# Optimization experiments

Hardware: AMD Instinct MI355X
Metric: run time of the kernel (lower is better)

Reference implementation:

```python
import jax, jax.numpy as jnp
import numpy as np

N_NODES = 100000
N_EDGES = 1600000
D_IN = 64
D_OUT = 64
ROW_WINDOW = 16  # TCGNN row-window size (metadata only)


def setup_inputs() -> dict:
    key = jax.random.key(0)
    ks = jax.random.split(key, 7)
    X = jax.random.normal(ks[0], (N_NODES, D_IN), dtype=jnp.float32)
    weights = jax.random.normal(ks[1], (D_IN, D_OUT), dtype=jnp.float32)
    # CSR row pointers: sorted offsets into the edge list, endpoints pinned.
    rp = jnp.sort(jax.random.randint(ks[2], (N_NODES + 1,), 0, N_EDGES, dtype=jnp.int32))
    row_pointers = rp.at[0].set(0).at[-1].set(N_EDGES)
    column_index = jax.random.randint(ks[3], (N_EDGES,), 0, N_NODES, dtype=jnp.int32)
    # TCGNN tiling metadata (does not affect the math; kept for signature fidelity)
    blockPartition = jax.random.randint(ks[4], (N_NODES // ROW_WINDOW,), 0, 8, dtype=jnp.int32)
    edgeToColumn = jax.random.randint(ks[5], (N_EDGES,), 0, N_NODES, dtype=jnp.int32)
    edgeToRow = jax.random.randint(ks[6], (N_EDGES,), 0, N_NODES, dtype=jnp.int32)
    return {
        "X": X,
        "weights": weights,
        "row_pointers": row_pointers,
        "column_index": column_index,
        "blockPartition": blockPartition,
        "edgeToColumn": edgeToColumn,
        "edgeToRow": edgeToRow,
    }


def reference(X, weights, row_pointers, column_index, blockPartition, edgeToColumn, edgeToRow):
    # TCGNN.forward == unweighted CSR SpMM: X_prime[i] = sum_{j in N(i)} X[j]
    n_edges = column_index.shape[0]
    # Map each edge position to its CSR row id.
    row_ids = jnp.searchsorted(row_pointers, jnp.arange(n_edges, dtype=row_pointers.dtype), side="right") - 1
    gathered = X[column_index]  # [n_edges, d_in] irregular gather
    X_prime = jax.ops.segment_sum(gathered, row_ids, num_segments=X.shape[0])  # [n_nodes, d_in]
    return X_prime @ weights  # dense GEMM [n_nodes, d_out]
```

## Files before the change

### kernel.cpp

```cpp
#include <hip/hip_runtime.h>
#include <cstdint>
#include <cstddef>

#define D 64

typedef float    f32x4 __attribute__((ext_vector_type(4)));
typedef short    s16x8 __attribute__((ext_vector_type(8)));
typedef uint32_t u32x4 __attribute__((ext_vector_type(4)));

__device__ __forceinline__ uint32_t rne_bf16(float f) {
    uint32_t x = __float_as_uint(f);
    return (x + 0x7fffu + ((x >> 16) & 1u)) >> 16;
}
__device__ __forceinline__ float bf16lo(uint32_t u) { return __uint_as_float(u << 16); }
__device__ __forceinline__ float bf16hi(uint32_t u) { return __uint_as_float(u & 0xffff0000u); }

__global__ __launch_bounds__(256) void xw_gemm_kernel(
    const float* __restrict__ X, const float* __restrict__ W,
    uint32_t* __restrict__ XWh, int n_nodes)
{
    const int lane = threadIdx.x & 63;
    const int n = lane & 15;
    const int q = lane >> 4;

    s16x8 Af[4][2];
#pragma unroll
    for (int c = 0; c < 4; ++c)
#pragma unroll
        for (int kb = 0; kb < 2; ++kb) {
            s16x8 af;
#pragma unroll
            for (int j = 0; j < 8; ++j) {
                const int k = kb * 32 + q * 8 + j;
                af[j] = (short)rne_bf16(W[k * D + c * 16 + n]);
            }
            Af[c][kb] = af;
        }

    const int n_tiles = (n_nodes + 15) / 16;
    const int gwave = (int)((blockIdx.x * blockDim.x + threadIdx.x) >> 6);
    const int nwaves = (int)((gridDim.x * blockDim.x) >> 6);

    for (int t = gwave; t < n_tiles; t += nwaves) {
        const int m0 = t * 16;
        int arow = m0 + n;
        if (arow >= n_nodes) arow = n_nodes - 1;
        const float* xp = X + (size_t)arow * D;

        s16x8 Bf[2];
#pragma unroll
        for (int kb = 0; kb < 2; ++kb) {
            const f32x4 x0 = __builtin_nontemporal_load((const f32x4*)(xp + kb * 32 + q * 8));
            const f32x4 x1 = __builtin_nontemporal_load((const f32x4*)(xp + kb * 32 + q * 8 + 4));
            s16x8 b;
            b[0] = (short)rne_bf16(x0.x); b[1] = (short)rne_bf16(x0.y);
            b[2] = (short)rne_bf16(x0.z); b[3] = (short)rne_bf16(x0.w);
            b[4] = (short)rne_bf16(x1.x); b[5] = (short)rne_bf16(x1.y);
            b[6] = (short)rne_bf16(x1.z); b[7] = (short)rne_bf16(x1.w);
            Bf[kb] = b;
        }

        const bool live = (m0 + n) < n_nodes;
#pragma unroll
        for (int c = 0; c < 4; ++c) {
            f32x4 z = {0.f, 0.f, 0.f, 0.f};
            z = __builtin_amdgcn_mfma_f32_16x16x32_bf16(Af[c][0], Bf[0], z, 0, 0, 0);
            z = __builtin_amdgcn_mfma_f32_16x16x32_bf16(Af[c][1], Bf[1], z, 0, 0, 0);
            if (live) {
                uint2 o;
                o.x = rne_bf16(z[0]) | (rne_bf16(z[1]) << 16);
                o.y = rne_bf16(z[2]) | (rne_bf16(z[3]) << 16);
                *(uint2*)(XWh + (size_t)(m0 + n) * 32 + c * 8 + q * 2) = o;
            }
        }
    }
}

__global__ __launch_bounds__(256) void gather1shot_kernel(
    const uint32_t* __restrict__ XWh, const int* __restrict__ rp,
    const int* __restrict__ ci, float* __restrict__ out, int n_nodes)
{
    const int lane = threadIdx.x & 63;
    const int o = lane >> 3;
    const int p = lane & 7;
    const int gw = (int)((blockIdx.x * blockDim.x + threadIdx.x) >> 6);
    const int row = __builtin_amdgcn_readfirstlane(gw);
    if (row >= n_nodes) return;

    const int e0 = rp[row];
    const int e1 = rp[row + 1];

    float acc[8] = {0, 0, 0, 0, 0, 0, 0, 0};

    int e = e0;
    while (e < e1) {
        const int rem = e1 - e;

        int idx[8];
        bool v[8];
#pragma unroll
        for (int t = 0; t < 8; ++t) {
            v[t] = (t * 8 + o) < rem;
            if (v[t]) idx[t] = ci[e + t * 8 + o];
        }
        u32x4 u[8];
#pragma unroll
        for (int t = 0; t < 8; ++t)
            if (v[t]) u[t] = *(const u32x4*)(XWh + (size_t)idx[t] * 32 + p * 4);
#pragma unroll
        for (int t = 0; t < 8; ++t) {
            if (v[t]) {
#pragma unroll
                for (int k = 0; k < 4; ++k) {
                    acc[2 * k]     += bf16lo(u[t][k]);
                    acc[2 * k + 1] += bf16hi(u[t][k]);
                }
            }
        }
        e += 64;
    }

#pragma unroll
    for (int j = 0; j < 8; ++j) {
        float vv = acc[j];
        vv += __shfl_xor(vv, 8, 64);
        vv += __shfl_xor(vv, 16, 64);
        vv += __shfl_xor(vv, 32, 64);
        acc[j] = vv;
    }
    if (lane < 8) {
        f32x4 w0 = {acc[0], acc[1], acc[2], acc[3]};
        f32x4 w1 = {acc[4], acc[5], acc[6], acc[7]};
        *(f32x4*)(out + (size_t)row * D + p * 8)     = w0;
        *(f32x4*)(out + (size_t)row * D + p * 8 + 4) = w1;
    }
}

__global__ __launch_bounds__(256) void fused_kernel(
    const float* __restrict__ X, const float* __restrict__ W,
    const int* __restrict__ rp, const int* __restrict__ ci,
    float* __restrict__ out, int n_nodes)
{
    __shared__ float Wl[D * D];
    for (int i = threadIdx.x; i < D * D; i += 256) Wl[i] = W[i];
    __syncthreads();

    const int lane = threadIdx.x & 63;
    const int gwave = (int)((blockIdx.x * blockDim.x + threadIdx.x) >> 6);
    const int nwaves = (int)((gridDim.x * blockDim.x) >> 6);

    for (int row = gwave; row < n_nodes; row += nwaves) {
        int e0 = rp[row];
        int e1 = rp[row + 1];
        float acc = 0.f;
        for (int e = e0; e < e1; ++e) acc += X[ci[e] * D + lane];
        float sum = 0.f;
#pragma unroll
        for (int d = 0; d < D; ++d) {
            float a = __shfl(acc, d, 64);
            sum += a * Wl[d * D + lane];
        }
        out[row * D + lane] = sum;
    }
}

extern "C" void kernel_launch(void* const* d_in, const int* in_sizes, int n_in,
                              void* d_out, int out_size, void* d_ws, size_t ws_size,
                              hipStream_t stream)
{
    const float* X  = (const float*)d_in[0];
    const float* W  = (const float*)d_in[1];
    const int*   rp = (const int*)d_in[2];
    const int*   ci = (const int*)d_in[3];
    float* out = (float*)d_out;

    const int n_nodes = in_sizes[2] - 1;
    const size_t row_bytes = 32 * sizeof(uint32_t);
    const size_t need = (size_t)n_nodes * row_bytes;

    if (ws_size >= need) {
        uint32_t* XWh = (uint32_t*)d_ws;

        xw_gemm_kernel<<<1024, 256, 0, stream>>>(X, W, XWh, n_nodes);

        const int gather_blocks = (n_nodes + 3) / 4;
        gather1shot_kernel<<<gather_blocks, 256, 0, stream>>>(XWh, rp, ci, out, n_nodes);
    } else {
        fused_kernel<<<2048, 256, 0, stream>>>(X, W, rp, ci, out, n_nodes);
    }
}
```

Baseline: 143.6 us.

## Make gather kernel persistent with next-row index prefetch and DPP reduction

Converts the one-wave-per-row gather kernel into a persistent kernel with a fixed grid that strides over rows. While the current row's feature gathers are in flight, it loads the next row's CSR bounds and first index chunk, aiming to hide the dependent index-load latency. The first cross-lane reduction step uses a DPP row rotate instead of a shuffle. In exchange it uses more registers and has fewer waves in flight, which may reduce memory-level parallelism on short rows.

```diff
diff --git a/kernel.cpp b/kernel.cpp
--- a/kernel.cpp
+++ b/kernel.cpp
@@ -14,6 +14,11 @@
 }
 __device__ __forceinline__ float bf16lo(uint32_t u) { return __uint_as_float(u << 16); }
 __device__ __forceinline__ float bf16hi(uint32_t u) { return __uint_as_float(u & 0xffff0000u); }
+
+__device__ __forceinline__ float dpp_xor8_add(float x) {
+    int y = __builtin_amdgcn_update_dpp(0, __float_as_int(x), 0x128, 0xF, 0xF, true);
+    return x + __int_as_float(y);
+}
 
 __global__ __launch_bounds__(256) void xw_gemm_kernel(
     const float* __restrict__ X, const float* __restrict__ W,
@@ -76,7 +81,7 @@
     }
 }
 
-__global__ __launch_bounds__(256) void gather1shot_kernel(
+__global__ __launch_bounds__(256) void gather_pers_kernel(
     const uint32_t* __restrict__ XWh, const int* __restrict__ rp,
     const int* __restrict__ ci, float* __restrict__ out, int n_nodes)
 {
@@ -84,29 +89,50 @@
     const int o = lane >> 3;
     const int p = lane & 7;
     const int gw = (int)((blockIdx.x * blockDim.x + threadIdx.x) >> 6);
-    const int row = __builtin_amdgcn_readfirstlane(gw);
+    const int nw = (int)((gridDim.x * blockDim.x) >> 6);
+
+    int row = __builtin_amdgcn_readfirstlane(gw);
     if (row >= n_nodes) return;
 
-    const int e0 = rp[row];
-    const int e1 = rp[row + 1];
-
-    float acc[8] = {0, 0, 0, 0, 0, 0, 0, 0};
-
-    int e = e0;
-    while (e < e1) {
-        const int rem = e1 - e;
-
-        int idx[8];
-        bool v[8];
+    int e0 = rp[row];
+    int e1 = rp[row + 1];
+    int idx[8];
+    bool v[8];
+    {
+        const int rem = e1 - e0;
 #pragma unroll
         for (int t = 0; t < 8; ++t) {
             v[t] = (t * 8 + o) < rem;
-            if (v[t]) idx[t] = ci[e + t * 8 + o];
-        }
+            if (v[t]) idx[t] = ci[e0 + t * 8 + o];
+        }
+    }
+
+    while (true) {
+        const int nrow = row + nw;
+        const bool have_next = nrow < n_nodes;
+
         u32x4 u[8];
 #pragma unroll
         for (int t = 0; t < 8; ++t)
             if (v[t]) u[t] = *(const u32x4*)(XWh + (size_t)idx[t] * 32 + p * 4);
+
+        int ne0 = 0, ne1 = 0;
+        int nidx[8];
+        bool nv[8];
+#pragma unroll
+        for (int t = 0; t < 8; ++t) nv[t] = false;
+        if (have_next) {
+            ne0 = rp[nrow];
+            ne1 = rp[nrow + 1];
+            const int nrem = ne1 - ne0;
+#pragma unroll
+            for (int t = 0; t < 8; ++t) {
+                nv[t] = (t * 8 + o) < nrem;
+                if (nv[t]) nidx[t] = ci[ne0 + t * 8 + o];
+            }
+        }
+
+        float acc[8] = {0, 0, 0, 0, 0, 0, 0, 0};
 #pragma unroll
         for (int t = 0; t < 8; ++t) {
             if (v[t]) {
@@ -117,22 +143,55 @@
                 }
             }
         }
-        e += 64;
-    }
-
-#pragma unroll
-    for (int j = 0; j < 8; ++j) {
-        float vv = acc[j];
-        vv += __shfl_xor(vv, 8, 64);
-        vv += __shfl_xor(vv, 16, 64);
-        vv += __shfl_xor(vv, 32, 64);
-        acc[j] = vv;
-    }
-    if (lane < 8) {
-        f32x4 w0 = {acc[0], acc[1], acc[2], acc[3]};
-        f32x4 w1 = {acc[4], acc[5], acc[6], acc[7]};
-        *(f32x4*)(out + (size_t)row * D + p * 8)     = w0;
-        *(f32x4*)(out + (size_t)row * D + p * 8 + 4) = w1;
+
+        for (int e = e0 + 64; e < e1; e += 64) {
+            const int rem2 = e1 - e;
+            int idx2[8];
+            bool v2[8];
+#pragma unroll
+            for (int t = 0; t < 8; ++t) {
+                v2[t] = (t * 8 + o) < rem2;
+                if (v2[t]) idx2[t] = ci[e + t * 8 + o];
+            }
+            u32x4 u2[8];
+#pragma unroll
+            for (int t = 0; t < 8; ++t)
+                if (v2[t]) u2[t] = *(const u32x4*)(XWh + (size_t)idx2[t] * 32 + p * 4);
+#pragma unroll
+            for (int t = 0; t < 8; ++t) {
+                if (v2[t]) {
+#pragma unroll
+                    for (int k = 0; k < 4; ++k) {
+                        acc[2 * k]     += bf16lo(u2[t][k]);
+                        acc[2 * k + 1] += bf16hi(u2[t][k]);
+                    }
+                }
+            }
+        }
+
+#pragma unroll
+        for (int j = 0; j < 8; ++j) {
+            float vv = dpp_xor8_add(acc[j]);
+            vv += __shfl_xor(vv, 16, 64);
+            vv += __shfl_xor(vv, 32, 64);
+            acc[j] = vv;
+        }
+        if (lane < 8) {
+            f32x4 w0 = {acc[0], acc[1], acc[2], acc[3]};
+            f32x4 w1 = {acc[4], acc[5], acc[6], acc[7]};
+            *(f32x4*)(out + (size_t)row * D + p * 8)     = w0;
+            *(f32x4*)(out + (size_t)row * D + p * 8 + 4) = w1;
+        }
+
+        if (!have_next) break;
+        row = nrow;
+        e0 = ne0;
+        e1 = ne1;
+#pragma unroll
+        for (int t = 0; t < 8; ++t) {
+            v[t] = nv[t];
+            idx[t] = nidx[t];
+        }
     }
 }
 
@@ -183,8 +242,7 @@
 
         xw_gemm_kernel<<<1024, 256, 0, stream>>>(X, W, XWh, n_nodes);
 
-        const int gather_blocks = (n_nodes + 3) / 4;
-        gather1shot_kernel<<<gather_blocks, 256, 0, stream>>>(XWh, rp, ci, out, n_nodes);
+        gather_pers_kernel<<<3072, 256, 0, stream>>>(XWh, rp, ci, out, n_nodes);
     } else {
         fused_kernel<<<2048, 256, 0, stream>>>(X, W, rp, ci, out, n_nodes);
     }
```

Measured after the change: 163.0 us. 1.14x slower.

## Map gather lanes to output features instead of edge-parallel with shuffle reduction

Applied to the files above, without the earlier changes.

The gather kernel now gives each lane one output feature and walks the row's edges one at a time. Each edge index is a wave-uniform scalar load, and every lane reads one dword from the bf16 row. This removes the cross-lane shuffle reduction and the per-edge validity masking of the old edge-parallel scheme. The cost is far less memory-level parallelism per row: with about 16 edges per row, the loop issues only about 8 loads in flight per wave, and each lane reads 4 bytes instead of a 16-byte vector.

```diff
diff --git a/kernel.cpp b/kernel.cpp
--- a/kernel.cpp
+++ b/kernel.cpp
@@ -12,8 +12,6 @@
     uint32_t x = __float_as_uint(f);
     return (x + 0x7fffu + ((x >> 16) & 1u)) >> 16;
 }
-__device__ __forceinline__ float bf16lo(uint32_t u) { return __uint_as_float(u << 16); }
-__device__ __forceinline__ float bf16hi(uint32_t u) { return __uint_as_float(u & 0xffff0000u); }
 
 __global__ __launch_bounds__(256) void xw_gemm_kernel(
     const float* __restrict__ X, const float* __restrict__ W,
@@ -76,13 +74,11 @@
     }
 }
 
-__global__ __launch_bounds__(256) void gather1shot_kernel(
+__global__ __launch_bounds__(256) void gather_feat_kernel(
     const uint32_t* __restrict__ XWh, const int* __restrict__ rp,
     const int* __restrict__ ci, float* __restrict__ out, int n_nodes)
 {
     const int lane = threadIdx.x & 63;
-    const int o = lane >> 3;
-    const int p = lane & 7;
     const int gw = (int)((blockIdx.x * blockDim.x + threadIdx.x) >> 6);
     const int row = __builtin_amdgcn_readfirstlane(gw);
     if (row >= n_nodes) return;
@@ -90,50 +86,30 @@
     const int e0 = rp[row];
     const int e1 = rp[row + 1];
 
-    float acc[8] = {0, 0, 0, 0, 0, 0, 0, 0};
+    const int dwoff = lane >> 1;
+    const uint32_t sh = (lane & 1) ? 0u : 16u;
+
+    float acc = 0.f;
 
     int e = e0;
-    while (e < e1) {
-        const int rem = e1 - e;
-
-        int idx[8];
-        bool v[8];
+    for (; e + 8 <= e1; e += 8) {
+        uint32_t u[8];
 #pragma unroll
         for (int t = 0; t < 8; ++t) {
-            v[t] = (t * 8 + o) < rem;
-            if (v[t]) idx[t] = ci[e + t * 8 + o];
+            const int idx = __builtin_amdgcn_readfirstlane(ci[e + t]);
+            u[t] = XWh[(size_t)idx * 32 + dwoff];
         }
-        u32x4 u[8];
 #pragma unroll
         for (int t = 0; t < 8; ++t)
-            if (v[t]) u[t] = *(const u32x4*)(XWh + (size_t)idx[t] * 32 + p * 4);
-#pragma unroll
-        for (int t = 0; t < 8; ++t) {
-            if (v[t]) {
-#pragma unroll
-                for (int k = 0; k < 4; ++k) {
-                    acc[2 * k]     += bf16lo(u[t][k]);
-                    acc[2 * k + 1] += bf16hi(u[t][k]);
-                }
-            }
-        }
-        e += 64;
+            acc += __uint_as_float((u[t] << sh) & 0xffff0000u);
+    }
+    for (; e < e1; ++e) {
+        const int idx = __builtin_amdgcn_readfirstlane(ci[e]);
+        const uint32_t u = XWh[(size_t)idx * 32 + dwoff];
+        acc += __uint_as_float((u << sh) & 0xffff0000u);
     }
 
-#pragma unroll
-    for (int j = 0; j < 8; ++j) {
-        float vv = acc[j];
-        vv += __shfl_xor(vv, 8, 64);
-        vv += __shfl_xor(vv, 16, 64);
-        vv += __shfl_xor(vv, 32, 64);
-        acc[j] = vv;
-    }
-    if (lane < 8) {
-        f32x4 w0 = {acc[0], acc[1], acc[2], acc[3]};
-        f32x4 w1 = {acc[4], acc[5], acc[6], acc[7]};
-        *(f32x4*)(out + (size_t)row * D + p * 8)     = w0;
-        *(f32x4*)(out + (size_t)row * D + p * 8 + 4) = w1;
-    }
+    out[(size_t)row * D + lane] = acc;
 }
 
 __global__ __launch_bounds__(256) void fused_kernel(
@@ -184,7 +160,7 @@
         xw_gemm_kernel<<<1024, 256, 0, stream>>>(X, W, XWh, n_nodes);
 
         const int gather_blocks = (n_nodes + 3) / 4;
-        gather1shot_kernel<<<gather_blocks, 256, 0, stream>>>(XWh, rp, ci, out, n_nodes);
+        gather_feat_kernel<<<gather_blocks, 256, 0, stream>>>(XWh, rp, ci, out, n_nodes);
     } else {
         fused_kernel<<<2048, 256, 0, stream>>>(X, W, rp, ci, out, n_nodes);
     }
```

Result: slower. 154.3 us (+7.5%).
